# Kernel optimization log

Hardware: AMD Instinct MI355X
Metric: run time of the kernel (lower is better)

## Reference

```python
import jax, jax.numpy as jnp
import numpy as np

B, C, H, W = 2, 4, 256, 256   # x shape; H == W == num_classes
NH = 2                         # num_heads
NC = 256                       # num_classes
CT = C * 256                   # conv output channels (dim * 16 * 16)
NCR = NC // 16                 # MLP reduced dim


def setup_inputs() -> dict:
    key = jax.random.key(0)
    ks = jax.random.split(key, 16)
    s = 0.02

    def n(k, shape):
        return jax.random.normal(k, shape, jnp.float32) * s

    inp = {
        "x": jax.random.normal(ks[0], (B, C, H, W), jnp.float32),
        "conv_w": n(ks[1], (CT, C, 3, 3)),          # OIHW
        "conv_b": jnp.zeros((CT,), jnp.float32),
        # MLP weights stored (in, out) so y = x @ W + b  (== torch Linear)
        "qW1": n(ks[2], (NC, NCR)), "qb1": jnp.zeros((NCR,), jnp.float32),
        "qW2": n(ks[3], (NC, NCR)), "qb2": jnp.zeros((NCR,), jnp.float32),
        "kW1": n(ks[4], (NC, NCR)), "kb1": jnp.zeros((NCR,), jnp.float32),
        "kW2": n(ks[5], (NC, NCR)), "kb2": jnp.zeros((NCR,), jnp.float32),
        "vW1": n(ks[6], (NC, NCR)), "vb1": jnp.zeros((NCR,), jnp.float32),
        "vW2": n(ks[7], (NC, NCR)), "vb2": jnp.zeros((NCR,), jnp.float32),
        "temperature": jnp.ones((NH * NH, 1, 1), jnp.float32),
    }
    return inp


def _mlp(x, W1, b1, W2, b2):
    # Linear+sigmoid on last dim (w), transpose, Linear+sigmoid on (h), transpose back
    x = jax.nn.sigmoid(x @ W1 + b1)      # (b, ct, h, w//16)
    x = jnp.swapaxes(x, 2, 3)            # (b, ct, w//16, h)
    x = jax.nn.sigmoid(x @ W2 + b2)      # (b, ct, w//16, h//16)
    return jnp.swapaxes(x, 2, 3)         # (b, ct, h//16, w//16)


def _to_heads(a, nh):
    # einops: 'b c (h head1) (w head2) -> b (head1 head2) c (h w)'
    bb, ct, ht, wt = a.shape
    a = a.reshape(bb, ct, ht // nh, nh, wt // nh, nh)
    a = a.transpose(0, 3, 5, 1, 2, 4)    # (b, head1, head2, c, h, w)
    return a.reshape(bb, nh * nh, ct, (ht // nh) * (wt // nh))


def reference(x, conv_w, conv_b, qW1, qb1, qW2, qb2, kW1, kb1, kW2, kb2,
              vW1, vb1, vW2, vb2, temperature):
    b, c, h, w = x.shape
    t = jax.lax.conv_general_dilated(
        x, conv_w, window_strides=(1, 1), padding=((1, 1), (1, 1)),
        dimension_numbers=("NCHW", "OIHW", "NCHW")) + conv_b[None, :, None, None]
    q = _to_heads(_mlp(t, qW1, qb1, qW2, qb2), NH)   # (b, nh^2, ct, hw')
    k = _to_heads(_mlp(t, kW1, kb1, kW2, kb2), NH)
    v = _to_heads(_mlp(t, vW1, vb1, vW2, vb2), NH)
    scores = jnp.einsum('bncx,bnex->bnce', q, k) * temperature  # (b, nh^2, ct, ct)
    p = jax.nn.softmax(scores, axis=-1)
    att = jnp.einsum('bnce,bnex->bncx', p, v)                   # (b, nh^2, ct, hw')
    return att.reshape(b, c, h, w)
```

## Files before the change

### kernel.cpp

```cpp
#include <hip/hip_runtime.h>
#include <cstdint>

constexpr int NB  = 2;
constexpr int NCI = 4;
constexpr int NHH = 256;
constexpr int NWW = 256;
constexpr int NCT = 1024;

constexpr size_t SW1F = 0;
constexpr size_t U16_BASE_F = 48;
constexpr size_t GP_U  = 0;
constexpr size_t CW_U  = 297216;
constexpr size_t W2T_U = 338176;
constexpr size_t QU_O  = 350464;
constexpr size_t KU_O  = 874752;
constexpr size_t VT_O  = 1399040;

typedef __attribute__((ext_vector_type(8))) short bf16x8;
typedef __attribute__((ext_vector_type(4))) float f32x4;

__device__ __forceinline__ uint16_t f2bf(float x) {
  uint32_t u = __float_as_uint(x);
  return (uint16_t)((u + 0x7FFFu + ((u >> 16) & 1u)) >> 16);
}
__device__ __forceinline__ uint32_t pk2bf(float a, float b) {
  const uint32_t au = __float_as_uint(a) + 0x8000u;
  const uint32_t bu = __float_as_uint(b) + 0x8000u;
  return __builtin_amdgcn_perm(bu, au, 0x07060302u);
}
__device__ __forceinline__ float sigmoid_f(float v) {
  return __builtin_amdgcn_rcpf(1.0f + __expf(-v));
}

__global__ __launch_bounds__(64) void k1_G(
    const float* __restrict__ x,
    const float* __restrict__ qW1, const float* __restrict__ kW1,
    const float* __restrict__ vW1,
    const float* __restrict__ conv_w,
    const float* __restrict__ qW2, const float* __restrict__ kW2,
    const float* __restrict__ vW2,
    float* __restrict__ wsf, uint16_t* __restrict__ wsu) {
  const int tid = threadIdx.x;
  const int NBLK = 3 * NB * NCI * (NHH / 4);
  int bid = blockIdx.x;

  if (bid >= NBLK + 3 + 64) {
    const int m = bid - (NBLK + 3 + 64);
    const float* W2 = (m == 0) ? qW2 : (m == 1) ? kW2 : vW2;
    for (int u = 0; u < 64; ++u) {
      const int idx = tid * 64 + u;
      const int s = idx >> 8, h = idx & 255;
      wsu[W2T_U + (size_t)m * 4096 + s * 256 + h] = f2bf(W2[h * 16 + s]);
    }
    return;
  }
  if (bid >= NBLK + 3) {
    const int p = bid - (NBLK + 3);
    const int o = p * 16 + (tid >> 2);
    const int ks = (tid & 3) * 10;
    for (int u = 0; u < 10; ++u) {
      const int k = ks + u;
      wsu[CW_U + (size_t)o * 40 + k] = (k < 36) ? f2bf(conv_w[o * 36 + k]) : (uint16_t)0;
    }
    return;
  }
  if (bid >= NBLK) {
    int m = bid - NBLK;
    if (tid < 16) {
      const float* W1 = (m == 0) ? qW1 : (m == 1) ? kW1 : vW1;
      float s = 0.f;
      for (int w = 0; w < 256; ++w) s += W1[w * 16 + tid];
      wsf[SW1F + m * 16 + tid] = s;
    }
    return;
  }

  const int m  = bid / (NB * NCI * (NHH / 4));
  int rem      = bid % (NB * NCI * (NHH / 4));
  const int b  = rem / (NCI * (NHH / 4));
  rem          = rem % (NCI * (NHH / 4));
  const int i  = rem / (NHH / 4);
  const int h0 = (rem % (NHH / 4)) * 4;
  const int mb = m * NB + b;

  const float* W1 = (m == 0) ? qW1 : (m == 1) ? kW1 : vW1;

  __shared__ float W1l[16 * 260];
  __shared__ float xlb[4][260];

  for (int idx4 = tid; idx4 < 1024; idx4 += 64) {
    const float4 t = ((const float4*)W1)[idx4];
    const int w = idx4 >> 2, r0 = (idx4 & 3) * 4;
    W1l[(r0 + 0) * 260 + w] = t.x;
    W1l[(r0 + 1) * 260 + w] = t.y;
    W1l[(r0 + 2) * 260 + w] = t.z;
    W1l[(r0 + 3) * 260 + w] = t.w;
  }
  const float* xbase = x + ((size_t)(b * NCI + i) * NHH + h0) * NWW;
  for (int idx = tid; idx < 4 * 256; idx += 64) {
    const int rr = idx >> 8, w = idx & 255;
    xlb[rr][1 + w] = xbase[rr * NWW + w];
  }
  if (tid < 4) {
    xlb[tid][0] = 0.f; xlb[tid][257] = 0.f; xlb[tid][258] = 0.f; xlb[tid][259] = 0.f;
  }
  __syncthreads();

  if (h0 == 0 && tid < 48) {
    const int dxp = tid >> 4, rp = tid & 15;
    wsu[GP_U + ((size_t)((mb * 4 + i) * 3 + dxp) * 16 + rp) * 258 + 0] = 0;
  }
  if (h0 == 252 && tid < 48) {
    const int dxp = tid >> 4, rp = tid & 15;
    wsu[GP_U + ((size_t)((mb * 4 + i) * 3 + dxp) * 16 + rp) * 258 + 257] = 0;
  }

  const int wc = tid >> 4, r = tid & 15;
  const int w0 = wc * 64;
  const size_t gb0 = GP_U + ((size_t)((mb * 4 + i) * 3 + 0) * 16 + r) * 258;

  #pragma unroll
  for (int rr = 0; rr < 4; ++rr) {
    const float* xl = xlb[rr];
    float a0 = 0.f, a1 = 0.f, a2 = 0.f;
    float4 cur = *(const float4*)&xl[w0];
    #pragma unroll 4
    for (int w = w0; w < w0 + 64; w += 4) {
      const float4 nxt = *(const float4*)&xl[w + 4];
      const float4 w1  = *(const float4*)&W1l[r * 260 + w];
      a0 += w1.x * cur.x + w1.y * cur.y + w1.z * cur.z + w1.w * cur.w;
      a1 += w1.x * cur.y + w1.y * cur.z + w1.z * cur.w + w1.w * nxt.x;
      a2 += w1.x * cur.z + w1.y * cur.w + w1.z * nxt.x + w1.w * nxt.y;
      cur = nxt;
    }
    a0 += __shfl_xor(a0, 16, 64); a0 += __shfl_xor(a0, 32, 64);
    a1 += __shfl_xor(a1, 16, 64); a1 += __shfl_xor(a1, 32, 64);
    a2 += __shfl_xor(a2, 16, 64); a2 += __shfl_xor(a2, 32, 64);
    if (wc == 0) {
      const int hp = 1 + h0 + rr;
      wsu[gb0 + hp]        = f2bf(a0);
      wsu[gb0 + 4128 + hp] = f2bf(a1);
      wsu[gb0 + 8256 + hp] = f2bf(a2);
    }
  }
}

__global__ __launch_bounds__(256, 4) void k2_mfma(
    const uint16_t* __restrict__ gp, const uint16_t* __restrict__ cwbf,
    const uint16_t* __restrict__ w2t,
    const float* __restrict__ conv_b,
    const float* __restrict__ qb1, const float* __restrict__ kb1, const float* __restrict__ vb1,
    const float* __restrict__ qb2, const float* __restrict__ kb2, const float* __restrict__ vb2,
    const float* __restrict__ wsf, uint16_t* __restrict__ wsu) {
  const int tid = threadIdx.x;
  const int bid = blockIdx.x;
  const int r  = bid & 15;
  const int og = (bid >> 4) & 15;
  const int mb = bid >> 8;
  const int m  = mb >> 1, b = mb & 1;

  const int wv  = tid >> 6;
  const int l   = tid & 63;
  const int l15 = l & 15;
  const int lg  = l >> 4;

  __shared__ uint16_t GS[256 * 40];
  __shared__ uint16_t y1l[4][16 * 72];

  {
    const int h = tid;
    uint16_t* gsrow = &GS[h * 40];
    #pragma unroll
    for (int i = 0; i < 4; ++i) {
      #pragma unroll
      for (int dx = 0; dx < 3; ++dx) {
        const uint16_t* g = gp + ((size_t)((mb * 4 + i) * 3 + dx) * 16 + r) * 258 + h;
        gsrow[i * 9 + 0 * 3 + dx] = g[0];
        gsrow[i * 9 + 1 * 3 + dx] = g[1];
        gsrow[i * 9 + 2 * 3 + dx] = g[2];
      }
    }
    gsrow[36] = 0; gsrow[37] = 0; gsrow[38] = 0; gsrow[39] = 0;
  }
  __syncthreads();

  const float* b1 = (m == 0) ? qb1 : (m == 1) ? kb1 : vb1;
  const float* b2 = (m == 0) ? qb2 : (m == 1) ? kb2 : vb2;

  const int o_blk = og * 64 + wv * 16;

  const uint16_t* cwrow = cwbf + (size_t)(o_blk + l15) * 40;
  bf16x8 cw0 = *(const bf16x8*)(cwrow + lg * 8);
  bf16x8 cw1 = {0,0,0,0,0,0,0,0};
  if (lg == 0) cw1 = *(const bf16x8*)(cwrow + 32);

  const uint16_t* w2row = w2t + (size_t)m * 4096 + (size_t)l15 * 256 + lg * 8;
  bf16x8 w2f0 = *(const bf16x8*)(w2row + 0 * 32);
  bf16x8 w2f1 = *(const bf16x8*)(w2row + 1 * 32);
  bf16x8 w2f2 = *(const bf16x8*)(w2row + 2 * 32);
  bf16x8 w2f3 = *(const bf16x8*)(w2row + 3 * 32);
  bf16x8 w2f4 = *(const bf16x8*)(w2row + 4 * 32);
  bf16x8 w2f5 = *(const bf16x8*)(w2row + 5 * 32);
  bf16x8 w2f6 = *(const bf16x8*)(w2row + 6 * 32);
  bf16x8 w2f7 = *(const bf16x8*)(w2row + 7 * 32);

  const float sw1r = wsf[SW1F + m * 16 + r];
  const float b1r  = b1[r];
  const float cbv  = conv_b[o_blk + l15];
  const float bias1 = cbv * sw1r + b1r;
  const float b2v  = b2[l15];

  uint16_t* yw = &y1l[wv][0];
  f32x4 acc2 = {0.f, 0.f, 0.f, 0.f};

  #pragma unroll
  for (int cc = 0; cc < 4; ++cc) {
    #pragma unroll
    for (int ct = 0; ct < 4; ++ct) {
      const uint16_t* arow = &GS[(cc * 64 + ct * 16 + l15) * 40];
      bf16x8 a0 = *(const bf16x8*)(arow + lg * 8);
      bf16x8 a1 = {0,0,0,0,0,0,0,0};
      if (lg == 0) a1 = *(const bf16x8*)(arow + 32);
      f32x4 d = {0.f, 0.f, 0.f, 0.f};
      d = __builtin_amdgcn_mfma_f32_16x16x32_bf16(a0, cw0, d, 0, 0, 0);
      d = __builtin_amdgcn_mfma_f32_16x16x32_bf16(a1, cw1, d, 0, 0, 0);
      const float y0 = sigmoid_f(d[0] + bias1);
      const float y1 = sigmoid_f(d[1] + bias1);
      const float y2 = sigmoid_f(d[2] + bias1);
      const float y3 = sigmoid_f(d[3] + bias1);
      uint32_t* yd = (uint32_t*)&yw[l15 * 72 + ct * 16 + lg * 4];
      yd[0] = pk2bf(y0, y1);
      yd[1] = pk2bf(y2, y3);
    }
    {
      const uint16_t* yrow = &yw[l15 * 72 + lg * 8];
      bf16x8 ya0 = *(const bf16x8*)(yrow + 0);
      bf16x8 ya1 = *(const bf16x8*)(yrow + 32);
      if (cc == 0) {
        acc2 = __builtin_amdgcn_mfma_f32_16x16x32_bf16(ya0, w2f0, acc2, 0, 0, 0);
        acc2 = __builtin_amdgcn_mfma_f32_16x16x32_bf16(ya1, w2f1, acc2, 0, 0, 0);
      } else if (cc == 1) {
        acc2 = __builtin_amdgcn_mfma_f32_16x16x32_bf16(ya0, w2f2, acc2, 0, 0, 0);
        acc2 = __builtin_amdgcn_mfma_f32_16x16x32_bf16(ya1, w2f3, acc2, 0, 0, 0);
      } else if (cc == 2) {
        acc2 = __builtin_amdgcn_mfma_f32_16x16x32_bf16(ya0, w2f4, acc2, 0, 0, 0);
        acc2 = __builtin_amdgcn_mfma_f32_16x16x32_bf16(ya1, w2f5, acc2, 0, 0, 0);
      } else {
        acc2 = __builtin_amdgcn_mfma_f32_16x16x32_bf16(ya0, w2f6, acc2, 0, 0, 0);
        acc2 = __builtin_amdgcn_mfma_f32_16x16x32_bf16(ya1, w2f7, acc2, 0, 0, 0);
      }
    }
  }

  const int s   = l15;
  const int n   = (s & 1) * 2 + (r & 1);
  const int xsp = (s >> 1) * 8 + (r >> 1);
  const int bn  = b * 4 + n;
  uint16_t* qk = wsu + ((m == 0) ? QU_O : KU_O);
  uint16_t* vT = wsu + VT_O;
  #pragma unroll
  for (int p = 0; p < 4; ++p) {
    const int o = o_blk + lg * 4 + p;
    const uint16_t y2 = f2bf(sigmoid_f(acc2[p] + b2v));
    if (m == 2) vT[((size_t)bn * 64 + xsp) * 1024 + o] = y2;
    else        qk[((size_t)bn * 1024 + o) * 64 + xsp] = y2;
  }
}

__global__ __launch_bounds__(512, 2) void k3_attn(
    const uint16_t* __restrict__ qu, const uint16_t* __restrict__ ku,
    const uint16_t* __restrict__ vtu, const float* __restrict__ temp,
    float* __restrict__ out) {
  const int tid = threadIdx.x;
  const int wv  = tid >> 6;
  const int l   = tid & 63;
  const int l15 = l & 15, lg = l >> 4;
  const int bn = blockIdx.x >> 6;
  const int ct = blockIdx.x & 63;
  const int cbase = ct * 16;
  const float tscale = temp[bn & 3];

  __shared__ __align__(16) char SH[36864];
  uint16_t* plw = (uint16_t*)SH + wv * 2304;
  float* poS = (float*)SH;
  float* mlS = poS + 8704;

  const uint16_t* qrow = qu + (size_t)(bn * 1024 + cbase + l15) * 64 + lg * 8;
  const bf16x8 qf0 = *(const bf16x8*)(qrow);
  const bf16x8 qf1 = *(const bf16x8*)(qrow + 32);

  const uint16_t* kb = ku  + (size_t)bn * 65536 + lg * 8;
  const uint16_t* vb = vtu + (size_t)bn * 65536 + lg * 8;

  f32x4 o0 = {0.f,0.f,0.f,0.f}, o1 = o0, o2 = o0, o3 = o0;
  float mrun = -3.0e38f, lrun = 0.f;

  #pragma unroll
  for (int et = 0; et < 2; ++et) {
    const int e0 = wv * 128 + et * 64;
    uint16_t* pl = plw + (et & 1) * 1152;

    f32x4 s0 = {0.f,0.f,0.f,0.f}, s1 = s0, s2 = s0, s3 = s0;
    {
      const uint16_t* kr0 = kb + (size_t)(e0 +  0 + l15) * 64;
      const uint16_t* kr1 = kb + (size_t)(e0 + 16 + l15) * 64;
      const uint16_t* kr2 = kb + (size_t)(e0 + 32 + l15) * 64;
      const uint16_t* kr3 = kb + (size_t)(e0 + 48 + l15) * 64;
      const bf16x8 ka0 = *(const bf16x8*)(kr0);
      const bf16x8 kb0 = *(const bf16x8*)(kr0 + 32);
      const bf16x8 ka1 = *(const bf16x8*)(kr1);
      const bf16x8 kb1_ = *(const bf16x8*)(kr1 + 32);
      const bf16x8 ka2 = *(const bf16x8*)(kr2);
      const bf16x8 kb2_ = *(const bf16x8*)(kr2 + 32);
      const bf16x8 ka3 = *(const bf16x8*)(kr3);
      const bf16x8 kb3_ = *(const bf16x8*)(kr3 + 32);
      s0 = __builtin_amdgcn_mfma_f32_16x16x32_bf16(ka0, qf0, s0, 0,0,0);
      s0 = __builtin_amdgcn_mfma_f32_16x16x32_bf16(kb0, qf1, s0, 0,0,0);
      s1 = __builtin_amdgcn_mfma_f32_16x16x32_bf16(ka1, qf0, s1, 0,0,0);
      s1 = __builtin_amdgcn_mfma_f32_16x16x32_bf16(kb1_, qf1, s1, 0,0,0);
      s2 = __builtin_amdgcn_mfma_f32_16x16x32_bf16(ka2, qf0, s2, 0,0,0);
      s2 = __builtin_amdgcn_mfma_f32_16x16x32_bf16(kb2_, qf1, s2, 0,0,0);
      s3 = __builtin_amdgcn_mfma_f32_16x16x32_bf16(ka3, qf0, s3, 0,0,0);
      s3 = __builtin_amdgcn_mfma_f32_16x16x32_bf16(kb3_, qf1, s3, 0,0,0);
    }
    #pragma unroll
    for (int p = 0; p < 4; ++p) {
      s0[p] *= tscale; s1[p] *= tscale; s2[p] *= tscale; s3[p] *= tscale;
    }

    float t0 = fmaxf(fmaxf(s0[0], s0[1]), fmaxf(s0[2], s0[3]));
    float t1 = fmaxf(fmaxf(s1[0], s1[1]), fmaxf(s1[2], s1[3]));
    float t2 = fmaxf(fmaxf(s2[0], s2[1]), fmaxf(s2[2], s2[3]));
    float t3 = fmaxf(fmaxf(s3[0], s3[1]), fmaxf(s3[2], s3[3]));
    float tmax = fmaxf(fmaxf(t0, t1), fmaxf(t2, t3));
    tmax = fmaxf(tmax, __shfl_xor(tmax, 16, 64));
    tmax = fmaxf(tmax, __shfl_xor(tmax, 32, 64));
    const float mnew = fmaxf(mrun, tmax);
    const float scl  = __expf(mrun - mnew);
    float psum = 0.f;
    #pragma unroll
    for (int p = 0; p < 4; ++p) { s0[p] = __expf(s0[p] - mnew); psum += s0[p]; }
    #pragma unroll
    for (int p = 0; p < 4; ++p) { s1[p] = __expf(s1[p] - mnew); psum += s1[p]; }
    #pragma unroll
    for (int p = 0; p < 4; ++p) { s2[p] = __expf(s2[p] - mnew); psum += s2[p]; }
    #pragma unroll
    for (int p = 0; p < 4; ++p) { s3[p] = __expf(s3[p] - mnew); psum += s3[p]; }
    psum += __shfl_xor(psum, 16, 64);
    psum += __shfl_xor(psum, 32, 64);
    lrun = lrun * scl + psum;
    mrun = mnew;

    {
      uint32_t* p0w = (uint32_t*)&pl[l15 * 72 +  0 + lg * 4];
      uint32_t* p1w = (uint32_t*)&pl[l15 * 72 + 16 + lg * 4];
      uint32_t* p2w = (uint32_t*)&pl[l15 * 72 + 32 + lg * 4];
      uint32_t* p3w = (uint32_t*)&pl[l15 * 72 + 48 + lg * 4];
      p0w[0] = pk2bf(s0[0], s0[1]); p0w[1] = pk2bf(s0[2], s0[3]);
      p1w[0] = pk2bf(s1[0], s1[1]); p1w[1] = pk2bf(s1[2], s1[3]);
      p2w[0] = pk2bf(s2[0], s2[1]); p2w[1] = pk2bf(s2[2], s2[3]);
      p3w[0] = pk2bf(s3[0], s3[1]); p3w[1] = pk2bf(s3[2], s3[3]);
    }

    #pragma unroll
    for (int p = 0; p < 4; ++p) {
      o0[p] *= scl; o1[p] *= scl; o2[p] *= scl; o3[p] *= scl;
    }

    {
      const bf16x8 pb0 = *(const bf16x8*)&pl[l15 * 72 +  0 + lg * 8];
      const bf16x8 pb1 = *(const bf16x8*)&pl[l15 * 72 + 32 + lg * 8];
      const uint16_t* vr0 = vb + (size_t)( 0 + l15) * 1024 + e0;
      const uint16_t* vr1 = vb + (size_t)(16 + l15) * 1024 + e0;
      const uint16_t* vr2 = vb + (size_t)(32 + l15) * 1024 + e0;
      const uint16_t* vr3 = vb + (size_t)(48 + l15) * 1024 + e0;
      bf16x8 va;
      va = *(const bf16x8*)(vr0);      o0 = __builtin_amdgcn_mfma_f32_16x16x32_bf16(va, pb0, o0, 0,0,0);
      va = *(const bf16x8*)(vr0 + 32); o0 = __builtin_amdgcn_mfma_f32_16x16x32_bf16(va, pb1, o0, 0,0,0);
      va = *(const bf16x8*)(vr1);      o1 = __builtin_amdgcn_mfma_f32_16x16x32_bf16(va, pb0, o1, 0,0,0);
      va = *(const bf16x8*)(vr1 + 32); o1 = __builtin_amdgcn_mfma_f32_16x16x32_bf16(va, pb1, o1, 0,0,0);
      va = *(const bf16x8*)(vr2);      o2 = __builtin_amdgcn_mfma_f32_16x16x32_bf16(va, pb0, o2, 0,0,0);
      va = *(const bf16x8*)(vr2 + 32); o2 = __builtin_amdgcn_mfma_f32_16x16x32_bf16(va, pb1, o2, 0,0,0);
      va = *(const bf16x8*)(vr3);      o3 = __builtin_amdgcn_mfma_f32_16x16x32_bf16(va, pb0, o3, 0,0,0);
      va = *(const bf16x8*)(vr3 + 32); o3 = __builtin_amdgcn_mfma_f32_16x16x32_bf16(va, pb1, o3, 0,0,0);
    }
  }

  __syncthreads();

  {
    float* po = poS + wv * 1088 + l15 * 68 + lg * 4;
    *(f32x4*)&po[ 0] = o0;
    *(f32x4*)&po[16] = o1;
    *(f32x4*)&po[32] = o2;
    *(f32x4*)&po[48] = o3;
    if (lg == 0) {
      mlS[wv * 32 + l15]      = mrun;
      mlS[wv * 32 + 16 + l15] = lrun;
    }
  }
  __syncthreads();

  {
    const int c  = tid >> 5;
    const int x2 = (tid & 31) * 2;

    float m0 = mlS[0 * 32 + c], m1 = mlS[1 * 32 + c];
    float m2 = mlS[2 * 32 + c], m3 = mlS[3 * 32 + c];
    float m4 = mlS[4 * 32 + c], m5 = mlS[5 * 32 + c];
    float m6 = mlS[6 * 32 + c], m7 = mlS[7 * 32 + c];
    const float M = fmaxf(fmaxf(fmaxf(m0, m1), fmaxf(m2, m3)),
                          fmaxf(fmaxf(m4, m5), fmaxf(m6, m7)));
    const float c0 = __expf(m0 - M), c1 = __expf(m1 - M);
    const float c2 = __expf(m2 - M), c3 = __expf(m3 - M);
    const float c4 = __expf(m4 - M), c5 = __expf(m5 - M);
    const float c6 = __expf(m6 - M), c7 = __expf(m7 - M);
    const float L = c0 * mlS[0 * 32 + 16 + c] + c1 * mlS[1 * 32 + 16 + c]
                  + c2 * mlS[2 * 32 + 16 + c] + c3 * mlS[3 * 32 + 16 + c]
                  + c4 * mlS[4 * 32 + 16 + c] + c5 * mlS[5 * 32 + 16 + c]
                  + c6 * mlS[6 * 32 + 16 + c] + c7 * mlS[7 * 32 + 16 + c];
    const float rl = __builtin_amdgcn_rcpf(L);

    const float* pb = poS + c * 68 + x2;
    float a0 = 0.f, a1 = 0.f;
    a0 += c0 * pb[0 * 1088]; a1 += c0 * pb[0 * 1088 + 1];
    a0 += c1 * pb[1 * 1088]; a1 += c1 * pb[1 * 1088 + 1];
    a0 += c2 * pb[2 * 1088]; a1 += c2 * pb[2 * 1088 + 1];
    a0 += c3 * pb[3 * 1088]; a1 += c3 * pb[3 * 1088 + 1];
    a0 += c4 * pb[4 * 1088]; a1 += c4 * pb[4 * 1088 + 1];
    a0 += c5 * pb[5 * 1088]; a1 += c5 * pb[5 * 1088 + 1];
    a0 += c6 * pb[6 * 1088]; a1 += c6 * pb[6 * 1088 + 1];
    a0 += c7 * pb[7 * 1088]; a1 += c7 * pb[7 * 1088 + 1];

    const int C = cbase + c;
    float* ob = out + ((size_t)bn * 256 + (C >> 2)) * 256 + (C & 3) * 64 + x2;
    ob[0] = a0 * rl;
    ob[1] = a1 * rl;
  }
}

extern "C" void kernel_launch(void* const* d_in, const int* in_sizes, int n_in,
                              void* d_out, int out_size, void* d_ws, size_t ws_size,
                              hipStream_t stream) {
  (void)in_sizes; (void)n_in; (void)out_size; (void)ws_size;
  const float* x      = (const float*)d_in[0];
  const float* conv_w = (const float*)d_in[1];
  const float* conv_b = (const float*)d_in[2];
  const float* qW1 = (const float*)d_in[3];
  const float* qb1 = (const float*)d_in[4];
  const float* qW2 = (const float*)d_in[5];
  const float* qb2 = (const float*)d_in[6];
  const float* kW1 = (const float*)d_in[7];
  const float* kb1 = (const float*)d_in[8];
  const float* kW2 = (const float*)d_in[9];
  const float* kb2 = (const float*)d_in[10];
  const float* vW1 = (const float*)d_in[11];
  const float* vb1 = (const float*)d_in[12];
  const float* vW2 = (const float*)d_in[13];
  const float* vb2 = (const float*)d_in[14];
  const float* temp = (const float*)d_in[15];
  float* wsf = (float*)d_ws;
  uint16_t* wsu = (uint16_t*)(wsf + U16_BASE_F);
  float* out = (float*)d_out;

  k1_G<<<dim3(1606), dim3(64), 0, stream>>>(x, qW1, kW1, vW1,
      conv_w, qW2, kW2, vW2, wsf, wsu);
  k2_mfma<<<dim3(1536), dim3(256), 0, stream>>>(
      wsu + GP_U, wsu + CW_U, wsu + W2T_U, conv_b,
      qb1, kb1, vb1, qb2, kb2, vb2, wsf, wsu);
  k3_attn<<<dim3(512), dim3(512), 0, stream>>>(
      wsu + QU_O, wsu + KU_O, wsu + VT_O, temp, out);
}
```

Before: 49.07 us.

## Hoist K/V loads up front in attention kernel and swizzle block-to-head mapping

The two-iteration key-tile loop in the attention kernel is manually unrolled, with all K tiles and the first V tile loaded at kernel start and the second V tile loaded during the first softmax, so memory latency overlaps compute. The first tile's softmax skips the running-max rescale. The block index mapping now puts the head/batch index in the low bits, so neighbouring blocks work on different (b,n) slices. The P staging buffer is now reused instead of double-buffered. This raises register pressure, which could hurt occupancy under the 512x2 launch bounds.

Measured after the change: 47.60 us. 3.0% less time.

```diff
diff --git a/kernel.cpp b/kernel.cpp
--- a/kernel.cpp
+++ b/kernel.cpp
@@ -275,13 +275,14 @@
   const int wv  = tid >> 6;
   const int l   = tid & 63;
   const int l15 = l & 15, lg = l >> 4;
-  const int bn = blockIdx.x >> 6;
-  const int ct = blockIdx.x & 63;
+  const int bid = blockIdx.x;
+  const int bn = bid & 7;
+  const int ct = bid >> 3;
   const int cbase = ct * 16;
   const float tscale = temp[bn & 3];
 
   __shared__ __align__(16) char SH[36864];
-  uint16_t* plw = (uint16_t*)SH + wv * 2304;
+  uint16_t* pl  = (uint16_t*)SH + wv * 2304;
   float* poS = (float*)SH;
   float* mlS = poS + 8704;
 
@@ -291,43 +292,74 @@
 
   const uint16_t* kb = ku  + (size_t)bn * 65536 + lg * 8;
   const uint16_t* vb = vtu + (size_t)bn * 65536 + lg * 8;
+  const int e0a = wv * 128, e0b = e0a + 64;
+
+  const uint16_t* ka_r0 = kb + (size_t)(e0a +  0 + l15) * 64;
+  const uint16_t* ka_r1 = kb + (size_t)(e0a + 16 + l15) * 64;
+  const uint16_t* ka_r2 = kb + (size_t)(e0a + 32 + l15) * 64;
+  const uint16_t* ka_r3 = kb + (size_t)(e0a + 48 + l15) * 64;
+  const bf16x8 k0a = *(const bf16x8*)(ka_r0);
+  const bf16x8 k0b = *(const bf16x8*)(ka_r0 + 32);
+  const bf16x8 k1a = *(const bf16x8*)(ka_r1);
+  const bf16x8 k1b = *(const bf16x8*)(ka_r1 + 32);
+  const bf16x8 k2a = *(const bf16x8*)(ka_r2);
+  const bf16x8 k2b = *(const bf16x8*)(ka_r2 + 32);
+  const bf16x8 k3a = *(const bf16x8*)(ka_r3);
+  const bf16x8 k3b = *(const bf16x8*)(ka_r3 + 32);
+
+  const uint16_t* kb_r0 = kb + (size_t)(e0b +  0 + l15) * 64;
+  const uint16_t* kb_r1 = kb + (size_t)(e0b + 16 + l15) * 64;
+  const uint16_t* kb_r2 = kb + (size_t)(e0b + 32 + l15) * 64;
+  const uint16_t* kb_r3 = kb + (size_t)(e0b + 48 + l15) * 64;
+  const bf16x8 k4a = *(const bf16x8*)(kb_r0);
+  const bf16x8 k4b = *(const bf16x8*)(kb_r0 + 32);
+  const bf16x8 k5a = *(const bf16x8*)(kb_r1);
+  const bf16x8 k5b = *(const bf16x8*)(kb_r1 + 32);
+  const bf16x8 k6a = *(const bf16x8*)(kb_r2);
+  const bf16x8 k6b = *(const bf16x8*)(kb_r2 + 32);
+  const bf16x8 k7a = *(const bf16x8*)(kb_r3);
+  const bf16x8 k7b = *(const bf16x8*)(kb_r3 + 32);
+
+  const uint16_t* vr0 = vb + (size_t)( 0 + l15) * 1024;
+  const uint16_t* vr1 = vb + (size_t)(16 + l15) * 1024;
+  const uint16_t* vr2 = vb + (size_t)(32 + l15) * 1024;
+  const uint16_t* vr3 = vb + (size_t)(48 + l15) * 1024;
+  const bf16x8 v0a = *(const bf16x8*)(vr0 + e0a);
+  const bf16x8 v0b = *(const bf16x8*)(vr0 + e0a + 32);
+  const bf16x8 v1a = *(const bf16x8*)(vr1 + e0a);
+  const bf16x8 v1b = *(const bf16x8*)(vr1 + e0a + 32);
+  const bf16x8 v2a = *(const bf16x8*)(vr2 + e0a);
+  const bf16x8 v2b = *(const bf16x8*)(vr2 + e0a + 32);
+  const bf16x8 v3a = *(const bf16x8*)(vr3 + e0a);
+  const bf16x8 v3b = *(const bf16x8*)(vr3 + e0a + 32);
 
   f32x4 o0 = {0.f,0.f,0.f,0.f}, o1 = o0, o2 = o0, o3 = o0;
-  float mrun = -3.0e38f, lrun = 0.f;
-
-  #pragma unroll
-  for (int et = 0; et < 2; ++et) {
-    const int e0 = wv * 128 + et * 64;
-    uint16_t* pl = plw + (et & 1) * 1152;
-
-    f32x4 s0 = {0.f,0.f,0.f,0.f}, s1 = s0, s2 = s0, s3 = s0;
-    {
-      const uint16_t* kr0 = kb + (size_t)(e0 +  0 + l15) * 64;
-      const uint16_t* kr1 = kb + (size_t)(e0 + 16 + l15) * 64;
-      const uint16_t* kr2 = kb + (size_t)(e0 + 32 + l15) * 64;
-      const uint16_t* kr3 = kb + (size_t)(e0 + 48 + l15) * 64;
-      const bf16x8 ka0 = *(const bf16x8*)(kr0);
-      const bf16x8 kb0 = *(const bf16x8*)(kr0 + 32);
-      const bf16x8 ka1 = *(const bf16x8*)(kr1);
-      const bf16x8 kb1_ = *(const bf16x8*)(kr1 + 32);
-      const bf16x8 ka2 = *(const bf16x8*)(kr2);
-      const bf16x8 kb2_ = *(const bf16x8*)(kr2 + 32);
-      const bf16x8 ka3 = *(const bf16x8*)(kr3);
-      const bf16x8 kb3_ = *(const bf16x8*)(kr3 + 32);
-      s0 = __builtin_amdgcn_mfma_f32_16x16x32_bf16(ka0, qf0, s0, 0,0,0);
-      s0 = __builtin_amdgcn_mfma_f32_16x16x32_bf16(kb0, qf1, s0, 0,0,0);
-      s1 = __builtin_amdgcn_mfma_f32_16x16x32_bf16(ka1, qf0, s1, 0,0,0);
-      s1 = __builtin_amdgcn_mfma_f32_16x16x32_bf16(kb1_, qf1, s1, 0,0,0);
-      s2 = __builtin_amdgcn_mfma_f32_16x16x32_bf16(ka2, qf0, s2, 0,0,0);
-      s2 = __builtin_amdgcn_mfma_f32_16x16x32_bf16(kb2_, qf1, s2, 0,0,0);
-      s3 = __builtin_amdgcn_mfma_f32_16x16x32_bf16(ka3, qf0, s3, 0,0,0);
-      s3 = __builtin_amdgcn_mfma_f32_16x16x32_bf16(kb3_, qf1, s3, 0,0,0);
-    }
+  float mrun, lrun;
+
+  f32x4 s0 = {0.f,0.f,0.f,0.f}, s1 = s0, s2 = s0, s3 = s0;
+  s0 = __builtin_amdgcn_mfma_f32_16x16x32_bf16(k0a, qf0, s0, 0,0,0);
+  s0 = __builtin_amdgcn_mfma_f32_16x16x32_bf16(k0b, qf1, s0, 0,0,0);
+  s1 = __builtin_amdgcn_mfma_f32_16x16x32_bf16(k1a, qf0, s1, 0,0,0);
+  s1 = __builtin_amdgcn_mfma_f32_16x16x32_bf16(k1b, qf1, s1, 0,0,0);
+  s2 = __builtin_amdgcn_mfma_f32_16x16x32_bf16(k2a, qf0, s2, 0,0,0);
+  s2 = __builtin_amdgcn_mfma_f32_16x16x32_bf16(k2b, qf1, s2, 0,0,0);
+  s3 = __builtin_amdgcn_mfma_f32_16x16x32_bf16(k3a, qf0, s3, 0,0,0);
+  s3 = __builtin_amdgcn_mfma_f32_16x16x32_bf16(k3b, qf1, s3, 0,0,0);
+
+  const bf16x8 w0a = *(const bf16x8*)(vr0 + e0b);
+  const bf16x8 w0b = *(const bf16x8*)(vr0 + e0b + 32);
+  const bf16x8 w1a = *(const bf16x8*)(vr1 + e0b);
+  const bf16x8 w1b = *(const bf16x8*)(vr1 + e0b + 32);
+  const bf16x8 w2a = *(const bf16x8*)(vr2 + e0b);
+  const bf16x8 w2b = *(const bf16x8*)(vr2 + e0b + 32);
+  const bf16x8 w3a = *(const bf16x8*)(vr3 + e0b);
+  const bf16x8 w3b = *(const bf16x8*)(vr3 + e0b + 32);
+
+  {
     #pragma unroll
     for (int p = 0; p < 4; ++p) {
       s0[p] *= tscale; s1[p] *= tscale; s2[p] *= tscale; s3[p] *= tscale;
     }
-
     float t0 = fmaxf(fmaxf(s0[0], s0[1]), fmaxf(s0[2], s0[3]));
     float t1 = fmaxf(fmaxf(s1[0], s1[1]), fmaxf(s1[2], s1[3]));
     float t2 = fmaxf(fmaxf(s2[0], s2[1]), fmaxf(s2[2], s2[3]));
@@ -335,55 +367,104 @@
     float tmax = fmaxf(fmaxf(t0, t1), fmaxf(t2, t3));
     tmax = fmaxf(tmax, __shfl_xor(tmax, 16, 64));
     tmax = fmaxf(tmax, __shfl_xor(tmax, 32, 64));
+    const float mnew = tmax;
+    float psum = 0.f;
+    #pragma unroll
+    for (int p = 0; p < 4; ++p) { s0[p] = __expf(s0[p] - mnew); psum += s0[p]; }
+    #pragma unroll
+    for (int p = 0; p < 4; ++p) { s1[p] = __expf(s1[p] - mnew); psum += s1[p]; }
+    #pragma unroll
+    for (int p = 0; p < 4; ++p) { s2[p] = __expf(s2[p] - mnew); psum += s2[p]; }
+    #pragma unroll
+    for (int p = 0; p < 4; ++p) { s3[p] = __expf(s3[p] - mnew); psum += s3[p]; }
+    psum += __shfl_xor(psum, 16, 64);
+    psum += __shfl_xor(psum, 32, 64);
+    lrun = psum;
+    mrun = mnew;
+
+    uint32_t* p0w = (uint32_t*)&pl[l15 * 72 +  0 + lg * 4];
+    uint32_t* p1w = (uint32_t*)&pl[l15 * 72 + 16 + lg * 4];
+    uint32_t* p2w = (uint32_t*)&pl[l15 * 72 + 32 + lg * 4];
+    uint32_t* p3w = (uint32_t*)&pl[l15 * 72 + 48 + lg * 4];
+    p0w[0] = pk2bf(s0[0], s0[1]); p0w[1] = pk2bf(s0[2], s0[3]);
+    p1w[0] = pk2bf(s1[0], s1[1]); p1w[1] = pk2bf(s1[2], s1[3]);
+    p2w[0] = pk2bf(s2[0], s2[1]); p2w[1] = pk2bf(s2[2], s2[3]);
+    p3w[0] = pk2bf(s3[0], s3[1]); p3w[1] = pk2bf(s3[2], s3[3]);
+
+    const bf16x8 pb0 = *(const bf16x8*)&pl[l15 * 72 +  0 + lg * 8];
+    const bf16x8 pb1 = *(const bf16x8*)&pl[l15 * 72 + 32 + lg * 8];
+    o0 = __builtin_amdgcn_mfma_f32_16x16x32_bf16(v0a, pb0, o0, 0,0,0);
+    o0 = __builtin_amdgcn_mfma_f32_16x16x32_bf16(v0b, pb1, o0, 0,0,0);
+    o1 = __builtin_amdgcn_mfma_f32_16x16x32_bf16(v1a, pb0, o1, 0,0,0);
+    o1 = __builtin_amdgcn_mfma_f32_16x16x32_bf16(v1b, pb1, o1, 0,0,0);
+    o2 = __builtin_amdgcn_mfma_f32_16x16x32_bf16(v2a, pb0, o2, 0,0,0);
+    o2 = __builtin_amdgcn_mfma_f32_16x16x32_bf16(v2b, pb1, o2, 0,0,0);
+    o3 = __builtin_amdgcn_mfma_f32_16x16x32_bf16(v3a, pb0, o3, 0,0,0);
+    o3 = __builtin_amdgcn_mfma_f32_16x16x32_bf16(v3b, pb1, o3, 0,0,0);
+  }
+
+  {
+    f32x4 u0 = {0.f,0.f,0.f,0.f}, u1 = u0, u2 = u0, u3 = u0;
+    u0 = __builtin_amdgcn_mfma_f32_16x16x32_bf16(k4a, qf0, u0, 0,0,0);
+    u0 = __builtin_amdgcn_mfma_f32_16x16x32_bf16(k4b, qf1, u0, 0,0,0);
+    u1 = __builtin_amdgcn_mfma_f32_16x16x32_bf16(k5a, qf0, u1, 0,0,0);
+    u1 = __builtin_amdgcn_mfma_f32_16x16x32_bf16(k5b, qf1, u1, 0,0,0);
+    u2 = __builtin_amdgcn_mfma_f32_16x16x32_bf16(k6a, qf0, u2, 0,0,0);
+    u2 = __builtin_amdgcn_mfma_f32_16x16x32_bf16(k6b, qf1, u2, 0,0,0);
+    u3 = __builtin_amdgcn_mfma_f32_16x16x32_bf16(k7a, qf0, u3, 0,0,0);
+    u3 = __builtin_amdgcn_mfma_f32_16x16x32_bf16(k7b, qf1, u3, 0,0,0);
+
+    #pragma unroll
+    for (int p = 0; p < 4; ++p) {
+      u0[p] *= tscale; u1[p] *= tscale; u2[p] *= tscale; u3[p] *= tscale;
+    }
+    float t0 = fmaxf(fmaxf(u0[0], u0[1]), fmaxf(u0[2], u0[3]));
+    float t1 = fmaxf(fmaxf(u1[0], u1[1]), fmaxf(u1[2], u1[3]));
+    float t2 = fmaxf(fmaxf(u2[0], u2[1]), fmaxf(u2[2], u2[3]));
+    float t3 = fmaxf(fmaxf(u3[0], u3[1]), fmaxf(u3[2], u3[3]));
+    float tmax = fmaxf(fmaxf(t0, t1), fmaxf(t2, t3));
+    tmax = fmaxf(tmax, __shfl_xor(tmax, 16, 64));
+    tmax = fmaxf(tmax, __shfl_xor(tmax, 32, 64));
     const float mnew = fmaxf(mrun, tmax);
     const float scl  = __expf(mrun - mnew);
     float psum = 0.f;
     #pragma unroll
-    for (int p = 0; p < 4; ++p) { s0[p] = __expf(s0[p] - mnew); psum += s0[p]; }
-    #pragma unroll
-    for (int p = 0; p < 4; ++p) { s1[p] = __expf(s1[p] - mnew); psum += s1[p]; }
-    #pragma unroll
-    for (int p = 0; p < 4; ++p) { s2[p] = __expf(s2[p] - mnew); psum += s2[p]; }
-    #pragma unroll
-    for (int p = 0; p < 4; ++p) { s3[p] = __expf(s3[p] - mnew); psum += s3[p]; }
+    for (int p = 0; p < 4; ++p) { u0[p] = __expf(u0[p] - mnew); psum += u0[p]; }
+    #pragma unroll
+    for (int p = 0; p < 4; ++p) { u1[p] = __expf(u1[p] - mnew); psum += u1[p]; }
+    #pragma unroll
+    for (int p = 0; p < 4; ++p) { u2[p] = __expf(u2[p] - mnew); psum += u2[p]; }
+    #pragma unroll
+    for (int p = 0; p < 4; ++p) { u3[p] = __expf(u3[p] - mnew); psum += u3[p]; }
     psum += __shfl_xor(psum, 16, 64);
     psum += __shfl_xor(psum, 32, 64);
     lrun = lrun * scl + psum;
     mrun = mnew;
 
-    {
-      uint32_t* p0w = (uint32_t*)&pl[l15 * 72 +  0 + lg * 4];
-      uint32_t* p1w = (uint32_t*)&pl[l15 * 72 + 16 + lg * 4];
-      uint32_t* p2w = (uint32_t*)&pl[l15 * 72 + 32 + lg * 4];
-      uint32_t* p3w = (uint32_t*)&pl[l15 * 72 + 48 + lg * 4];
-      p0w[0] = pk2bf(s0[0], s0[1]); p0w[1] = pk2bf(s0[2], s0[3]);
-      p1w[0] = pk2bf(s1[0], s1[1]); p1w[1] = pk2bf(s1[2], s1[3]);
-      p2w[0] = pk2bf(s2[0], s2[1]); p2w[1] = pk2bf(s2[2], s2[3]);
-      p3w[0] = pk2bf(s3[0], s3[1]); p3w[1] = pk2bf(s3[2], s3[3]);
-    }
+    uint32_t* p0w = (uint32_t*)&pl[l15 * 72 +  0 + lg * 4];
+    uint32_t* p1w = (uint32_t*)&pl[l15 * 72 + 16 + lg * 4];
+    uint32_t* p2w = (uint32_t*)&pl[l15 * 72 + 32 + lg * 4];
+    uint32_t* p3w = (uint32_t*)&pl[l15 * 72 + 48 + lg * 4];
+    p0w[0] = pk2bf(u0[0], u0[1]); p0w[1] = pk2bf(u0[2], u0[3]);
+    p1w[0] = pk2bf(u1[0], u1[1]); p1w[1] = pk2bf(u1[2], u1[3]);
+    p2w[0] = pk2bf(u2[0], u2[1]); p2w[1] = pk2bf(u2[2], u2[3]);
+    p3w[0] = pk2bf(u3[0], u3[1]); p3w[1] = pk2bf(u3[2], u3[3]);
 
     #pragma unroll
     for (int p = 0; p < 4; ++p) {
       o0[p] *= scl; o1[p] *= scl; o2[p] *= scl; o3[p] *= scl;
     }
 
-    {
-      const bf16x8 pb0 = *(const bf16x8*)&pl[l15 * 72 +  0 + lg * 8];
-      const bf16x8 pb1 = *(const bf16x8*)&pl[l15 * 72 + 32 + lg * 8];
-      const uint16_t* vr0 = vb + (size_t)( 0 + l15) * 1024 + e0;
-      const uint16_t* vr1 = vb + (size_t)(16 + l15) * 1024 + e0;
-      const uint16_t* vr2 = vb + (size_t)(32 + l15) * 1024 + e0;
-      const uint16_t* vr3 = vb + (size_t)(48 + l15) * 1024 + e0;
-      bf16x8 va;
-      va = *(const bf16x8*)(vr0);      o0 = __builtin_amdgcn_mfma_f32_16x16x32_bf16(va, pb0, o0, 0,0,0);
-      va = *(const bf16x8*)(vr0 + 32); o0 = __builtin_amdgcn_mfma_f32_16x16x32_bf16(va, pb1, o0, 0,0,0);
-      va = *(const bf16x8*)(vr1);      o1 = __builtin_amdgcn_mfma_f32_16x16x32_bf16(va, pb0, o1, 0,0,0);
-      va = *(const bf16x8*)(vr1 + 32); o1 = __builtin_amdgcn_mfma_f32_16x16x32_bf16(va, pb1, o1, 0,0,0);
-      va = *(const bf16x8*)(vr2);      o2 = __builtin_amdgcn_mfma_f32_16x16x32_bf16(va, pb0, o2, 0,0,0);
-      va = *(const bf16x8*)(vr2 + 32); o2 = __builtin_amdgcn_mfma_f32_16x16x32_bf16(va, pb1, o2, 0,0,0);
-      va = *(const bf16x8*)(vr3);      o3 = __builtin_amdgcn_mfma_f32_16x16x32_bf16(va, pb0, o3, 0,0,0);
-      va = *(const bf16x8*)(vr3 + 32); o3 = __builtin_amdgcn_mfma_f32_16x16x32_bf16(va, pb1, o3, 0,0,0);
-    }
+    const bf16x8 pb0 = *(const bf16x8*)&pl[l15 * 72 +  0 + lg * 8];
+    const bf16x8 pb1 = *(const bf16x8*)&pl[l15 * 72 + 32 + lg * 8];
+    o0 = __builtin_amdgcn_mfma_f32_16x16x32_bf16(w0a, pb0, o0, 0,0,0);
+    o0 = __builtin_amdgcn_mfma_f32_16x16x32_bf16(w0b, pb1, o0, 0,0,0);
+    o1 = __builtin_amdgcn_mfma_f32_16x16x32_bf16(w1a, pb0, o1, 0,0,0);
+    o1 = __builtin_amdgcn_mfma_f32_16x16x32_bf16(w1b, pb1, o1, 0,0,0);
+    o2 = __builtin_amdgcn_mfma_f32_16x16x32_bf16(w2a, pb0, o2, 0,0,0);
+    o2 = __builtin_amdgcn_mfma_f32_16x16x32_bf16(w2b, pb1, o2, 0,0,0);
+    o3 = __builtin_amdgcn_mfma_f32_16x16x32_bf16(w3a, pb0, o3, 0,0,0);
+    o3 = __builtin_amdgcn_mfma_f32_16x16x32_bf16(w3b, pb1, o3, 0,0,0);
   }
 
   __syncthreads();
```
